# Optimization experiments

Hardware: AMD Instinct MI355X
Metric: run time of the kernel (lower is better)

The kernel has to match this reference:

```python
import jax, jax.numpy as jnp
import numpy as np

TAU_MIN = 0.001
XPBD_ITERS = 4
XPBD_COMPLIANCE = 0.0
XPBD_MAX_CORR = 0.15

B, N, D, E = 4, 50000, 256, 800000


def setup_inputs() -> dict:
    key = jax.random.key(0)
    ks = jax.random.split(key, 7)
    keypoints = jax.random.normal(ks[0], (B, N, 3), dtype=jnp.float32)
    timesteps = jax.random.uniform(ks[1], (B,), dtype=jnp.float32)
    hand_tokens = jax.random.normal(ks[2], (B, N, D), dtype=jnp.float32)
    head_w = jax.random.normal(ks[3], (D, 3), dtype=jnp.float32) * 0.02
    head_b = jnp.zeros((3,), dtype=jnp.float32)
    edge_index = jax.random.randint(ks[4], (2, E), 0, N, dtype=jnp.int32)
    rest_lengths = jax.random.uniform(ks[5], (E,), dtype=jnp.float32) + 0.1
    return {
        "keypoints": keypoints,
        "timesteps": timesteps,
        "hand_tokens": hand_tokens,
        "head_w": head_w,
        "head_b": head_b,
        "edge_index": edge_index,
        "rest_lengths": rest_lengths,
    }


def _xpbd_project(x, src, dst, rest_lengths):
    # x: (B, N, 3); src/dst: (E,); rest_lengths: (E,)
    L0 = rest_lengths[None, :, None]          # (1, E, 1)
    w_i = 1.0                                  # inv_mass is None -> unit inverse masses
    w_j = 1.0
    alpha = XPBD_COMPLIANCE / (float(XPBD_ITERS) + 1e-08)
    denom = w_i + w_j + alpha + 1e-09
    for _ in range(XPBD_ITERS):
        diff = x[:, src] - x[:, dst]           # (B, E, 3) edge gather
        dist = jnp.linalg.norm(diff, axis=-1, keepdims=True)  # (B, E, 1)
        C = dist - L0
        n = diff / (dist + 1e-09)
        d_lambda = -C / denom
        correction = jnp.clip(d_lambda * n, -XPBD_MAX_CORR, XPBD_MAX_CORR)
        delta = (jnp.zeros_like(x)
                 .at[:, src].add(w_i * correction)
                 .at[:, dst].add(-w_j * correction))  # scatter-add back to nodes
        x = x + delta
    return x


def reference(keypoints, timesteps, hand_tokens, head_w, head_b, edge_index, rest_lengths):
    # tau = clamp(1 - t, min=tau_min), broadcast to (B, 1, 1)
    tau = jnp.maximum(1.0 - timesteps, TAU_MIN)[:, None, None]
    v_raw = hand_tokens @ head_w + head_b      # (B, N, 3) velocity head
    x_pred = keypoints + tau * v_raw
    src = edge_index[0]
    dst = edge_index[1]
    x_corrected = _xpbd_project(x_pred, src, dst, rest_lengths)
    v_eff = (x_corrected - keypoints) / tau
    return v_eff
```

## Files before the change

kernel.cpp:

```cpp
#include <hip/hip_runtime.h>

#define BB 4
#define NN 50000
#define DD 256
#define EE 800000
#define TAU_MIN_F 0.001f
#define MAX_CORR_F 0.15f

#define CAP 80
#define NPART 8
#define PNODES (NN / NPART)
#define PS_CE 2048
#define PS_NCHUNK ((EE + PS_CE - 1) / PS_CE)

#define XPB 2048
#define S1_GRID (XPB + NPART * PS_NCHUNK)
#define NWAVE (XPB * 4)

__global__ __launch_bounds__(256) void stage1_kernel(
    const float* __restrict__ kp, const float* __restrict__ ts,
    const float* __restrict__ ht, const float* __restrict__ hw,
    const float* __restrict__ hb, float4* __restrict__ x,
    const int* __restrict__ ei, const float* __restrict__ L0,
    int* __restrict__ counts, int2* __restrict__ adj)
{
    if ((int)blockIdx.x >= XPB) {
        const int pb    = (int)blockIdx.x - XPB;
        const int part  = pb & 7;
        const int chunk = pb >> 3;
        const int lo   = part * PNODES;
        const int hi   = lo + PNODES;
        const int base = chunk * PS_CE;
        const int eEnd = min(base + PS_CE, EE);
        for (int e = base + (int)threadIdx.x; e < eEnd; e += 256) {
            const int s = ei[e];
            const int d = ei[EE + e];
            const int r = __float_as_int(L0[e]);
            if (s >= lo && s < hi) {
                const int p = atomicAdd(&counts[s], 1);
                if (p < CAP) adj[s * CAP + p] = make_int2(d << 2, r);
            }
            if (d >= lo && d < hi) {
                const int p = atomicAdd(&counts[d], 1);
                if (p < CAP) adj[d * CAP + p] = make_int2(s << 2, r);
            }
        }
        return;
    }

    const int lane = threadIdx.x & 63;
    const int wave = ((int)blockIdx.x * 256 + (int)threadIdx.x) >> 6;
    const int d0   = lane * 4;

    float W[4][3];
#pragma unroll
    for (int j = 0; j < 4; ++j)
#pragma unroll
        for (int k = 0; k < 3; ++k)
            W[j][k] = hw[(d0 + j) * 3 + k];
    const float b0 = hb[0], b1 = hb[1], b2 = hb[2];

    int i = wave;
    for (; i + NWAVE < BB * NN; i += 2 * NWAVE) {
        const int iA = i, iB = i + NWAVE;
        const int rowA = (iA & 3) * NN + (iA >> 2);
        const int rowB = (iB & 3) * NN + (iB >> 2);
        const float4 hA = *(const float4*)(ht + (size_t)rowA * DD + d0);
        const float4 hB = *(const float4*)(ht + (size_t)rowB * DD + d0);
        float aA0 = hA.x * W[0][0] + hA.y * W[1][0] + hA.z * W[2][0] + hA.w * W[3][0];
        float aA1 = hA.x * W[0][1] + hA.y * W[1][1] + hA.z * W[2][1] + hA.w * W[3][1];
        float aA2 = hA.x * W[0][2] + hA.y * W[1][2] + hA.z * W[2][2] + hA.w * W[3][2];
        float aB0 = hB.x * W[0][0] + hB.y * W[1][0] + hB.z * W[2][0] + hB.w * W[3][0];
        float aB1 = hB.x * W[0][1] + hB.y * W[1][1] + hB.z * W[2][1] + hB.w * W[3][1];
        float aB2 = hB.x * W[0][2] + hB.y * W[1][2] + hB.z * W[2][2] + hB.w * W[3][2];
#pragma unroll
        for (int off = 32; off > 0; off >>= 1) {
            aA0 += __shfl_down(aA0, off);
            aB0 += __shfl_down(aB0, off);
            aA1 += __shfl_down(aA1, off);
            aB1 += __shfl_down(aB1, off);
            aA2 += __shfl_down(aA2, off);
            aB2 += __shfl_down(aB2, off);
        }
        if (lane == 0) {
            {
                const int bA = iA & 3;
                const float tau = fmaxf(1.0f - ts[bA], TAU_MIN_F);
                float4 v;
                v.x = kp[rowA * 3 + 0] + tau * (aA0 + b0);
                v.y = kp[rowA * 3 + 1] + tau * (aA1 + b1);
                v.z = kp[rowA * 3 + 2] + tau * (aA2 + b2);
                v.w = 0.0f;
                x[iA] = v;
            }
            {
                const int bB = iB & 3;
                const float tau = fmaxf(1.0f - ts[bB], TAU_MIN_F);
                float4 v;
                v.x = kp[rowB * 3 + 0] + tau * (aB0 + b0);
                v.y = kp[rowB * 3 + 1] + tau * (aB1 + b1);
                v.z = kp[rowB * 3 + 2] + tau * (aB2 + b2);
                v.w = 0.0f;
                x[iB] = v;
            }
        }
    }
    if (i < BB * NN) {
        const int row = (i & 3) * NN + (i >> 2);
        const float4 h = *(const float4*)(ht + (size_t)row * DD + d0);
        float a0 = h.x * W[0][0] + h.y * W[1][0] + h.z * W[2][0] + h.w * W[3][0];
        float a1 = h.x * W[0][1] + h.y * W[1][1] + h.z * W[2][1] + h.w * W[3][1];
        float a2 = h.x * W[0][2] + h.y * W[1][2] + h.z * W[2][2] + h.w * W[3][2];
#pragma unroll
        for (int off = 32; off > 0; off >>= 1) {
            a0 += __shfl_down(a0, off);
            a1 += __shfl_down(a1, off);
            a2 += __shfl_down(a2, off);
        }
        if (lane == 0) {
            const int b = i & 3;
            const float tau = fmaxf(1.0f - ts[b], TAU_MIN_F);
            float4 v;
            v.x = kp[row * 3 + 0] + tau * (a0 + b0);
            v.y = kp[row * 3 + 1] + tau * (a1 + b1);
            v.z = kp[row * 3 + 2] + tau * (a2 + b2);
            v.w = 0.0f;
            x[i] = v;
        }
    }
}

__global__ __launch_bounds__(256) void gather_kernel(
    const float4* __restrict__ xin, float4* __restrict__ xout,
    const int* __restrict__ counts, const int2* __restrict__ adj,
    const float* __restrict__ kp, const float* __restrict__ ts,
    float* __restrict__ out, int final_iter)
{
    const int tid  = blockIdx.x * 256 + threadIdx.x;
    const int b    = tid & 3;
    const int sub  = (tid >> 2) & 7;
    const int node = tid >> 5;

    const float4 xc = xin[(node << 2) + b];
    float a0 = 0.0f, a1 = 0.0f, a2 = 0.0f;

    const int beg = node * CAP;
    const int end = beg + min(counts[node], CAP);

    int k = beg + sub;
    for (; k + 8 < end; k += 16) {
        const int2 e0 = adj[k];
        const int2 e1 = adj[k + 8];
        const float4 n0 = xin[e0.x + b];
        const float4 n1 = xin[e1.x + b];
        {
            const float dx = xc.x - n0.x, dy = xc.y - n0.y, dz = xc.z - n0.z;
            const float dist = sqrtf(dx * dx + dy * dy + dz * dz);
            const float s = (__int_as_float(e0.y) - dist) * 0.5f / (dist + 1e-9f);
            a0 += fminf(fmaxf(s * dx, -MAX_CORR_F), MAX_CORR_F);
            a1 += fminf(fmaxf(s * dy, -MAX_CORR_F), MAX_CORR_F);
            a2 += fminf(fmaxf(s * dz, -MAX_CORR_F), MAX_CORR_F);
        }
        {
            const float dx = xc.x - n1.x, dy = xc.y - n1.y, dz = xc.z - n1.z;
            const float dist = sqrtf(dx * dx + dy * dy + dz * dz);
            const float s = (__int_as_float(e1.y) - dist) * 0.5f / (dist + 1e-9f);
            a0 += fminf(fmaxf(s * dx, -MAX_CORR_F), MAX_CORR_F);
            a1 += fminf(fmaxf(s * dy, -MAX_CORR_F), MAX_CORR_F);
            a2 += fminf(fmaxf(s * dz, -MAX_CORR_F), MAX_CORR_F);
        }
    }
    if (k < end) {
        const int2 e0 = adj[k];
        const float4 n0 = xin[e0.x + b];
        const float dx = xc.x - n0.x, dy = xc.y - n0.y, dz = xc.z - n0.z;
        const float dist = sqrtf(dx * dx + dy * dy + dz * dz);
        const float s = (__int_as_float(e0.y) - dist) * 0.5f / (dist + 1e-9f);
        a0 += fminf(fmaxf(s * dx, -MAX_CORR_F), MAX_CORR_F);
        a1 += fminf(fmaxf(s * dy, -MAX_CORR_F), MAX_CORR_F);
        a2 += fminf(fmaxf(s * dz, -MAX_CORR_F), MAX_CORR_F);
    }

    a0 += __shfl_xor(a0, 4);  a0 += __shfl_xor(a0, 8);  a0 += __shfl_xor(a0, 16);
    a1 += __shfl_xor(a1, 4);  a1 += __shfl_xor(a1, 8);  a1 += __shfl_xor(a1, 16);
    a2 += __shfl_xor(a2, 4);  a2 += __shfl_xor(a2, 8);  a2 += __shfl_xor(a2, 16);

    if (sub == 0) {
        if (!final_iter) {
            float4 v; v.x = xc.x + a0; v.y = xc.y + a1; v.z = xc.z + a2; v.w = 0.0f;
            xout[(node << 2) + b] = v;
        } else {
            const int row = b * NN + node;
            const float tau = fmaxf(1.0f - ts[b], TAU_MIN_F);
            const float it  = 1.0f / tau;
            out[row * 3 + 0] = (xc.x + a0 - kp[row * 3 + 0]) * it;
            out[row * 3 + 1] = (xc.y + a1 - kp[row * 3 + 1]) * it;
            out[row * 3 + 2] = (xc.z + a2 - kp[row * 3 + 2]) * it;
        }
    }
}

extern "C" void kernel_launch(void* const* d_in, const int* in_sizes, int n_in,
                              void* d_out, int out_size, void* d_ws, size_t ws_size,
                              hipStream_t stream)
{
    const float* kp = (const float*)d_in[0];
    const float* ts = (const float*)d_in[1];
    const float* ht = (const float*)d_in[2];
    const float* hw = (const float*)d_in[3];
    const float* hb = (const float*)d_in[4];
    const int*   ei = (const int*)d_in[5];
    const float* L0 = (const float*)d_in[6];
    float* out = (float*)d_out;

    char* w = (char*)d_ws;
    int2*   adj    = (int2*)w;                 w += (size_t)NN * CAP * sizeof(int2);
    float4* xA     = (float4*)w;               w += (size_t)BB * NN * sizeof(float4);
    float4* xB     = (float4*)w;               w += (size_t)BB * NN * sizeof(float4);
    int*    counts = (int*)w;

    hipMemsetAsync(counts, 0, (size_t)NN * sizeof(int), stream);

    stage1_kernel<<<S1_GRID, 256, 0, stream>>>(kp, ts, ht, hw, hb, xA,
                                               ei, L0, counts, adj);

    const int gatherBlocks = (32 * NN) / 256;
    gather_kernel<<<gatherBlocks, 256, 0, stream>>>(xA, xB, counts, adj, kp, ts, out, 0);
    gather_kernel<<<gatherBlocks, 256, 0, stream>>>(xB, xA, counts, adj, kp, ts, out, 0);
    gather_kernel<<<gatherBlocks, 256, 0, stream>>>(xA, xB, counts, adj, kp, ts, out, 0);
    gather_kernel<<<gatherBlocks, 256, 0, stream>>>(xB, xA, counts, adj, kp, ts, out, 1);
}
```

Measured before the change: 438.6 us.

## Use DPP wave reductions, reorder bucket blocks, vectorize adjacency loads

Replaces the shuffle-down reductions in the velocity head with DPP row-shift/broadcast reductions, so the result lands in lane 63. Moves the edge-bucketing blocks to the front of the grid so they start before the projection blocks, and splits the bucketing atomics from the adjacency stores. In the gather kernel, each sub-lane now walks a contiguous segment of the node's adjacency list and loads two entries at once with an int4 load instead of strided int2 loads. The aim is cheaper reductions, better overlap of the atomic-heavy bucketing, and fewer memory transactions in the iterated gather. Contiguous segments can unbalance work across sub-lanes when counts are uneven.

```diff
diff --git a/kernel.cpp b/kernel.cpp
--- a/kernel.cpp
+++ b/kernel.cpp
@@ -12,10 +12,20 @@
 #define PNODES (NN / NPART)
 #define PS_CE 2048
 #define PS_NCHUNK ((EE + PS_CE - 1) / PS_CE)
-
+#define NBUCKET (NPART * PS_NCHUNK)
 #define XPB 2048
-#define S1_GRID (XPB + NPART * PS_NCHUNK)
+#define S1_GRID (NBUCKET + XPB)
 #define NWAVE (XPB * 4)
+
+__device__ __forceinline__ float wsum64(float x) {
+    x += __int_as_float(__builtin_amdgcn_update_dpp(0, __float_as_int(x), 0x111, 0xf, 0xf, true));
+    x += __int_as_float(__builtin_amdgcn_update_dpp(0, __float_as_int(x), 0x112, 0xf, 0xf, true));
+    x += __int_as_float(__builtin_amdgcn_update_dpp(0, __float_as_int(x), 0x114, 0xf, 0xf, true));
+    x += __int_as_float(__builtin_amdgcn_update_dpp(0, __float_as_int(x), 0x118, 0xf, 0xf, true));
+    x += __int_as_float(__builtin_amdgcn_update_dpp(0, __float_as_int(x), 0x142, 0xf, 0xf, true));
+    x += __int_as_float(__builtin_amdgcn_update_dpp(0, __float_as_int(x), 0x143, 0xf, 0xf, true));
+    return x;
+}
 
 __global__ __launch_bounds__(256) void stage1_kernel(
     const float* __restrict__ kp, const float* __restrict__ ts,
@@ -24,10 +34,9 @@
     const int* __restrict__ ei, const float* __restrict__ L0,
     int* __restrict__ counts, int2* __restrict__ adj)
 {
-    if ((int)blockIdx.x >= XPB) {
-        const int pb    = (int)blockIdx.x - XPB;
-        const int part  = pb & 7;
-        const int chunk = pb >> 3;
+    if ((int)blockIdx.x < NBUCKET) {
+        const int part  = (int)blockIdx.x & 7;
+        const int chunk = (int)blockIdx.x >> 3;
         const int lo   = part * PNODES;
         const int hi   = lo + PNODES;
         const int base = chunk * PS_CE;
@@ -36,20 +45,19 @@
             const int s = ei[e];
             const int d = ei[EE + e];
             const int r = __float_as_int(L0[e]);
-            if (s >= lo && s < hi) {
-                const int p = atomicAdd(&counts[s], 1);
-                if (p < CAP) adj[s * CAP + p] = make_int2(d << 2, r);
-            }
-            if (d >= lo && d < hi) {
-                const int p = atomicAdd(&counts[d], 1);
-                if (p < CAP) adj[d * CAP + p] = make_int2(s << 2, r);
-            }
+            const bool hs = (s >= lo) & (s < hi);
+            const bool hd = (d >= lo) & (d < hi);
+            int ps = CAP, pd = CAP;
+            if (hs) ps = atomicAdd(&counts[s], 1);
+            if (hd) pd = atomicAdd(&counts[d], 1);
+            if (hs && ps < CAP) adj[s * CAP + ps] = make_int2(d << 2, r);
+            if (hd && pd < CAP) adj[d * CAP + pd] = make_int2(s << 2, r);
         }
         return;
     }
 
     const int lane = threadIdx.x & 63;
-    const int wave = ((int)blockIdx.x * 256 + (int)threadIdx.x) >> 6;
+    const int wave = (((int)blockIdx.x - NBUCKET) * 256 + (int)threadIdx.x) >> 6;
     const int d0   = lane * 4;
 
     float W[4][3];
@@ -73,19 +81,12 @@
         float aB0 = hB.x * W[0][0] + hB.y * W[1][0] + hB.z * W[2][0] + hB.w * W[3][0];
         float aB1 = hB.x * W[0][1] + hB.y * W[1][1] + hB.z * W[2][1] + hB.w * W[3][1];
         float aB2 = hB.x * W[0][2] + hB.y * W[1][2] + hB.z * W[2][2] + hB.w * W[3][2];
-#pragma unroll
-        for (int off = 32; off > 0; off >>= 1) {
-            aA0 += __shfl_down(aA0, off);
-            aB0 += __shfl_down(aB0, off);
-            aA1 += __shfl_down(aA1, off);
-            aB1 += __shfl_down(aB1, off);
-            aA2 += __shfl_down(aA2, off);
-            aB2 += __shfl_down(aB2, off);
-        }
-        if (lane == 0) {
+        aA0 = wsum64(aA0);  aB0 = wsum64(aB0);
+        aA1 = wsum64(aA1);  aB1 = wsum64(aB1);
+        aA2 = wsum64(aA2);  aB2 = wsum64(aB2);
+        if (lane == 63) {
             {
-                const int bA = iA & 3;
-                const float tau = fmaxf(1.0f - ts[bA], TAU_MIN_F);
+                const float tau = fmaxf(1.0f - ts[iA & 3], TAU_MIN_F);
                 float4 v;
                 v.x = kp[rowA * 3 + 0] + tau * (aA0 + b0);
                 v.y = kp[rowA * 3 + 1] + tau * (aA1 + b1);
@@ -94,8 +95,7 @@
                 x[iA] = v;
             }
             {
-                const int bB = iB & 3;
-                const float tau = fmaxf(1.0f - ts[bB], TAU_MIN_F);
+                const float tau = fmaxf(1.0f - ts[iB & 3], TAU_MIN_F);
                 float4 v;
                 v.x = kp[rowB * 3 + 0] + tau * (aB0 + b0);
                 v.y = kp[rowB * 3 + 1] + tau * (aB1 + b1);
@@ -111,15 +111,9 @@
         float a0 = h.x * W[0][0] + h.y * W[1][0] + h.z * W[2][0] + h.w * W[3][0];
         float a1 = h.x * W[0][1] + h.y * W[1][1] + h.z * W[2][1] + h.w * W[3][1];
         float a2 = h.x * W[0][2] + h.y * W[1][2] + h.z * W[2][2] + h.w * W[3][2];
-#pragma unroll
-        for (int off = 32; off > 0; off >>= 1) {
-            a0 += __shfl_down(a0, off);
-            a1 += __shfl_down(a1, off);
-            a2 += __shfl_down(a2, off);
-        }
-        if (lane == 0) {
-            const int b = i & 3;
-            const float tau = fmaxf(1.0f - ts[b], TAU_MIN_F);
+        a0 = wsum64(a0);  a1 = wsum64(a1);  a2 = wsum64(a2);
+        if (lane == 63) {
+            const float tau = fmaxf(1.0f - ts[i & 3], TAU_MIN_F);
             float4 v;
             v.x = kp[row * 3 + 0] + tau * (a0 + b0);
             v.y = kp[row * 3 + 1] + tau * (a1 + b1);
@@ -145,18 +139,19 @@
     float a0 = 0.0f, a1 = 0.0f, a2 = 0.0f;
 
     const int beg = node * CAP;
-    const int end = beg + min(counts[node], CAP);
-
-    int k = beg + sub;
-    for (; k + 8 < end; k += 16) {
-        const int2 e0 = adj[k];
-        const int2 e1 = adj[k + 8];
-        const float4 n0 = xin[e0.x + b];
-        const float4 n1 = xin[e1.x + b];
+    const int cnt = min(counts[node], CAP);
+    const int seg = ((cnt + 15) >> 4) << 1;
+    int k        = beg + sub * seg;
+    const int ke = min(k + seg, beg + cnt);
+
+    for (; k + 1 < ke; k += 2) {
+        const int4 e = *(const int4*)(&adj[k]);
+        const float4 n0 = xin[e.x + b];
+        const float4 n1 = xin[e.z + b];
         {
             const float dx = xc.x - n0.x, dy = xc.y - n0.y, dz = xc.z - n0.z;
             const float dist = sqrtf(dx * dx + dy * dy + dz * dz);
-            const float s = (__int_as_float(e0.y) - dist) * 0.5f / (dist + 1e-9f);
+            const float s = (__int_as_float(e.y) - dist) * 0.5f / (dist + 1e-9f);
             a0 += fminf(fmaxf(s * dx, -MAX_CORR_F), MAX_CORR_F);
             a1 += fminf(fmaxf(s * dy, -MAX_CORR_F), MAX_CORR_F);
             a2 += fminf(fmaxf(s * dz, -MAX_CORR_F), MAX_CORR_F);
@@ -164,13 +159,13 @@
         {
             const float dx = xc.x - n1.x, dy = xc.y - n1.y, dz = xc.z - n1.z;
             const float dist = sqrtf(dx * dx + dy * dy + dz * dz);
-            const float s = (__int_as_float(e1.y) - dist) * 0.5f / (dist + 1e-9f);
+            const float s = (__int_as_float(e.w) - dist) * 0.5f / (dist + 1e-9f);
             a0 += fminf(fmaxf(s * dx, -MAX_CORR_F), MAX_CORR_F);
             a1 += fminf(fmaxf(s * dy, -MAX_CORR_F), MAX_CORR_F);
             a2 += fminf(fmaxf(s * dz, -MAX_CORR_F), MAX_CORR_F);
         }
     }
-    if (k < end) {
+    if (k < ke) {
         const int2 e0 = adj[k];
         const float4 n0 = xin[e0.x + b];
         const float dx = xc.x - n0.x, dy = xc.y - n0.y, dz = xc.z - n0.z;
```

Result: no change. 443.4 us (+1.1%).
